# Kernel optimization log

Measured on AMD Instinct MI355X. Metric: run time of the kernel, lower is better.

## Reference

```python
import jax, jax.numpy as jnp
import numpy as np

N = 50000          # num nodes
E = 800000         # num edges
IN0 = 768
# layer configs: (in_channels, out_channels, heads, concat)
CFG = [(768, 64, 4, True), (256, 64, 4, True), (256, 64, 1, False)]


def setup_inputs() -> dict:
    key = jax.random.key(0)
    ks = iter(jax.random.split(key, 80))
    def nrm(shape, fan_in):
        return jax.random.normal(next(ks), shape, jnp.float32) * (1.0 / np.sqrt(fan_in))
    inp = {}
    inp["edge_index"] = jax.random.randint(next(ks), (2, E), 0, N)
    inp["edge_attr"] = jax.random.normal(next(ks), (E, 1), jnp.float32)
    inp["x"] = jax.random.normal(next(ks), (N, IN0), jnp.float32) * 0.05  # node_embeddings param
    for i, (cin, cout, h, concat) in enumerate(CFG):
        hc = h * cout
        nd = hc if concat else cout
        inp[f"Wl{i}"] = nrm((hc, cin), cin)
        inp[f"bl{i}"] = jnp.zeros((hc,), jnp.float32)
        inp[f"Wr{i}"] = nrm((hc, cin), cin)
        inp[f"br{i}"] = jnp.zeros((hc,), jnp.float32)
        inp[f"We{i}"] = nrm((hc, 1), 1)          # lin_edge, edge_dim=1, no bias
        inp[f"att{i}"] = nrm((h, cout), cout)     # attention vector a
        inp[f"b{i}"] = jnp.zeros((nd,), jnp.float32)   # conv output bias
        inp[f"g{i}"] = jnp.ones((nd,), jnp.float32)    # LayerNorm gamma
        inp[f"beta{i}"] = jnp.zeros((nd,), jnp.float32)  # LayerNorm beta
    # residual projections (only where in_channels != norm_dim): layer0 768->256, layer2 256->64
    inp["Rw0"] = nrm((256, 768), 768)
    inp["Rb0"] = jnp.zeros((256,), jnp.float32)
    inp["Rw2"] = nrm((64, 256), 256)
    inp["Rb2"] = jnp.zeros((64,), jnp.float32)
    return inp


def _gatv2(x, edge_index, edge_attr, Wl, bl, Wr, br, We, att, bias, heads, cout, concat):
    n = x.shape[0]
    src, dst = edge_index[0], edge_index[1]
    xl = (x @ Wl.T + bl).reshape(n, heads, cout)   # source transform
    xr = (x @ Wr.T + br).reshape(n, heads, cout)   # target transform
    e = (edge_attr @ We.T).reshape(-1, heads, cout)
    z = jax.nn.leaky_relu(xl[src] + xr[dst] + e, 0.2)          # [E,H,C]
    logits = jnp.einsum('ehc,hc->eh', z, att)                  # [E,H]
    m = jax.ops.segment_max(logits, dst, num_segments=n)       # segment softmax over dst
    ex = jnp.exp(logits - m[dst])
    denom = jax.ops.segment_sum(ex, dst, num_segments=n)
    alpha = ex / denom[dst]                                    # [E,H]
    msg = xl[src] * alpha[..., None]                           # [E,H,C]
    out = jax.ops.segment_sum(msg, dst, num_segments=n)        # [N,H,C]
    out = out.reshape(n, heads * cout) if concat else out.mean(axis=1)
    return out + bias


def _ln(x, g, b, eps=1e-5):
    mu = x.mean(-1, keepdims=True)
    v = ((x - mu) ** 2).mean(-1, keepdims=True)
    return (x - mu) * jax.lax.rsqrt(v + eps) * g + b


def reference(edge_index, edge_attr, x,
              Wl0, bl0, Wr0, br0, We0, att0, b0, g0, beta0,
              Wl1, bl1, Wr1, br1, We1, att1, b1, g1, beta1,
              Wl2, bl2, Wr2, br2, We2, att2, b2, g2, beta2,
              Rw0, Rb0, Rw2, Rb2):
    # eval mode: attention dropout disabled. Returns final_embeddings (bottleneck is None).
    h = _gatv2(x, edge_index, edge_attr, Wl0, bl0, Wr0, br0, We0, att0, b0, 4, 64, True)
    h = jax.nn.leaky_relu(_ln(h, g0, beta0), 0.01) + (x @ Rw0.T + Rb0)
    h1 = _gatv2(h, edge_index, edge_attr, Wl1, bl1, Wr1, br1, We1, att1, b1, 4, 64, True)
    h1 = jax.nn.leaky_relu(_ln(h1, g1, beta1), 0.01) + h      # Identity residual
    h2 = _gatv2(h1, edge_index, edge_attr, Wl2, bl2, Wr2, br2, We2, att2, b2, 1, 64, False)
    h2 = jax.nn.leaky_relu(_ln(h2, g2, beta2), 0.01) + (h1 @ Rw2.T + Rb2)
    return h2
```

## Files before the change

### kernel.cpp

```cpp
#include <hip/hip_runtime.h>
#include <math.h>

static constexpr int NN = 50000;
static constexpr int NE = 800000;
static constexpr int MPAD = 50048;

typedef __attribute__((ext_vector_type(8))) __bf16 bf16x8;
typedef __attribute__((ext_vector_type(4))) __bf16 bf16x4;
typedef __attribute__((ext_vector_type(4))) float f32x4;
typedef __bf16 bf16_t;

__device__ __forceinline__ float leakyf(float x, float s) { return x > 0.f ? x : s * x; }

__global__ void k_count(const int* __restrict__ dst, int* __restrict__ cnt, int n) {
    int e = blockIdx.x * 256 + threadIdx.x;
    if (e < n) atomicAdd(&cnt[dst[e]], 1);
}

__global__ void k_scan1(const int* __restrict__ cnt, int* __restrict__ rp,
                        int* __restrict__ partials, int n) {
    __shared__ int sm[256];
    int tid = threadIdx.x;
    int i = blockIdx.x * 256 + tid;
    int v = (i < n) ? cnt[i] : 0;
    int x = v;
    sm[tid] = x;
    __syncthreads();
    for (int off = 1; off < 256; off <<= 1) {
        int t = (tid >= off) ? sm[tid - off] : 0;
        __syncthreads();
        x += t;
        sm[tid] = x;
        __syncthreads();
    }
    if (i < n) rp[i] = x - v;
    if (tid == 255) partials[blockIdx.x] = x;
}

__global__ void k_scan2(const int* __restrict__ partials, int* __restrict__ poffs, int nb) {
    __shared__ int sm[256];
    int tid = threadIdx.x;
    int v = (tid < nb) ? partials[tid] : 0;
    int x = v;
    sm[tid] = x;
    __syncthreads();
    for (int off = 1; off < 256; off <<= 1) {
        int t = (tid >= off) ? sm[tid - off] : 0;
        __syncthreads();
        x += t;
        sm[tid] = x;
        __syncthreads();
    }
    if (tid < nb) poffs[tid] = x - v;
}

__global__ void k_scan3(int* __restrict__ rp, const int* __restrict__ poffs,
                        int* __restrict__ woff, int n, int total) {
    int i = blockIdx.x * 256 + threadIdx.x;
    if (i < n) {
        int v = rp[i] + poffs[blockIdx.x];
        rp[i] = v;
        woff[i] = v;
    }
    if (i == 0) rp[n] = total;
}

__global__ void k_scatter(const int* __restrict__ srcA, const int* __restrict__ dstA,
                          const float* __restrict__ ea, int* __restrict__ woff,
                          int* __restrict__ csr_src, float* __restrict__ csr_ea, int n) {
    int e = blockIdx.x * 256 + threadIdx.x;
    if (e < n) {
        int d = dstA[e];
        int pos = atomicAdd(&woff[d], 1);
        csr_src[pos] = srcA[e];
        csr_ea[pos] = ea[e];
    }
}

__global__ void k_f2b(const float* __restrict__ s, bf16_t* __restrict__ d, int n) {
    for (int i = (blockIdx.x * 256 + threadIdx.x) * 8; i < n; i += gridDim.x * 256 * 8) {
        float4 a = *(const float4*)&s[i];
        float4 b = *(const float4*)&s[i + 4];
        bf16x8 o;
        o[0] = (__bf16)a.x; o[1] = (__bf16)a.y; o[2] = (__bf16)a.z; o[3] = (__bf16)a.w;
        o[4] = (__bf16)b.x; o[5] = (__bf16)b.y; o[6] = (__bf16)b.z; o[7] = (__bf16)b.w;
        *(bf16x8*)&d[i] = o;
    }
}

__global__ void k_f2bw(const float* s0, bf16_t* d0, int n0,
                       const float* s1, bf16_t* d1, int n1,
                       const float* s2, bf16_t* d2, int n2,
                       const float* s3, bf16_t* d3, int n3,
                       const float* s4, bf16_t* d4, int n4,
                       const float* s5, bf16_t* d5, int n5,
                       const float* s6, bf16_t* d6, int n6,
                       const float* s7, bf16_t* d7, int n7) {
    const float* s; bf16_t* d; int n;
    switch (blockIdx.y) {
        case 0: s = s0; d = d0; n = n0; break;
        case 1: s = s1; d = d1; n = n1; break;
        case 2: s = s2; d = d2; n = n2; break;
        case 3: s = s3; d = d3; n = n3; break;
        case 4: s = s4; d = d4; n = n4; break;
        case 5: s = s5; d = d5; n = n5; break;
        case 6: s = s6; d = d6; n = n6; break;
        default: s = s7; d = d7; n = n7; break;
    }
    for (int i = (blockIdx.x * 256 + threadIdx.x) * 8; i < n; i += gridDim.x * 256 * 8) {
        float4 a = *(const float4*)&s[i];
        float4 b = *(const float4*)&s[i + 4];
        bf16x8 o;
        o[0] = (__bf16)a.x; o[1] = (__bf16)a.y; o[2] = (__bf16)a.z; o[3] = (__bf16)a.w;
        o[4] = (__bf16)b.x; o[5] = (__bf16)b.y; o[6] = (__bf16)b.z; o[7] = (__bf16)b.w;
        *(bf16x8*)&d[i] = o;
    }
}

__global__ void k_catb(float* __restrict__ dst,
                       const float* s0, int o0, int n0, const float* s1, int o1, int n1,
                       const float* s2, int o2, int n2, const float* s3, int o3, int n3,
                       const float* s4, int o4, int n4, const float* s5, int o5, int n5,
                       const float* s6, int o6, int n6, const float* s7, int o7, int n7) {
    const float* s; int off, n;
    switch (blockIdx.x) {
        case 0: s = s0; off = o0; n = n0; break;
        case 1: s = s1; off = o1; n = n1; break;
        case 2: s = s2; off = o2; n = n2; break;
        case 3: s = s3; off = o3; n = n3; break;
        case 4: s = s4; off = o4; n = n4; break;
        case 5: s = s5; off = o5; n = n5; break;
        case 6: s = s6; off = o6; n = n6; break;
        default: s = s7; off = o7; n = n7; break;
    }
    int i = threadIdx.x;
    if (i < n) dst[off + i] = s[i];
}

template <int BN>
__global__ __launch_bounds__(256) void k_gemm_mfma(
    const bf16_t* __restrict__ A, const bf16_t* __restrict__ W,
    const float* __restrict__ bias, bf16_t* __restrict__ C,
    int Mpad, int Nc, int K) {
    constexpr int BM = 128;
    constexpr int FRN = BN / 32;
    constexpr int WN = BN / 2;
    constexpr int BCHW = BN / 64;

    __shared__ __align__(16) bf16_t As[BM * 32];
    __shared__ __align__(16) bf16_t Bs[BN * 32];

    const int tid = threadIdx.x;
    const int wid = tid >> 6;
    const int lane = tid & 63;
    const int wr = wid >> 1, wc = wid & 1;
    const int bm = blockIdx.x * BM;
    const int bn = blockIdx.y * BN;

    const int srow = lane >> 2;
    const int scol = (lane & 3) * 8;

    f32x4 acc[4][FRN];
#pragma unroll
    for (int m = 0; m < 4; ++m)
#pragma unroll
        for (int n = 0; n < FRN; ++n) acc[m][n] = (f32x4){0.f, 0.f, 0.f, 0.f};

    const bf16_t* ag[2];
#pragma unroll
    for (int j = 0; j < 2; ++j)
        ag[j] = A + (size_t)(bm + (wid * 2 + j) * 16 + srow) * K + scol;
    const bf16_t* bg[BCHW];
#pragma unroll
    for (int j = 0; j < BCHW; ++j)
        bg[j] = W + (size_t)(bn + (wid * BCHW + j) * 16 + srow) * K + scol;

    for (int k0 = 0; k0 < K; k0 += 32) {
#pragma unroll
        for (int j = 0; j < 2; ++j) {
            __builtin_amdgcn_global_load_lds(
                (const __attribute__((address_space(1))) void*)(ag[j] + k0),
                (__attribute__((address_space(3))) void*)(As + (wid * 2 + j) * 512),
                16, 0, 0);
        }
#pragma unroll
        for (int j = 0; j < BCHW; ++j) {
            __builtin_amdgcn_global_load_lds(
                (const __attribute__((address_space(1))) void*)(bg[j] + k0),
                (__attribute__((address_space(3))) void*)(Bs + (wid * BCHW + j) * 512),
                16, 0, 0);
        }
        __syncthreads();

        bf16x8 bfr[FRN];
#pragma unroll
        for (int n = 0; n < FRN; ++n)
            bfr[n] = *(const bf16x8*)&Bs[(wc * WN + n * 16 + (lane & 15)) * 32 + (lane >> 4) * 8];
        bf16x8 afr[4];
#pragma unroll
        for (int m = 0; m < 4; ++m)
            afr[m] = *(const bf16x8*)&As[(wr * 64 + m * 16 + (lane & 15)) * 32 + (lane >> 4) * 8];
#pragma unroll
        for (int m = 0; m < 4; ++m)
#pragma unroll
            for (int n = 0; n < FRN; ++n)
                acc[m][n] = __builtin_amdgcn_mfma_f32_16x16x32_bf16(afr[m], bfr[n], acc[m][n], 0, 0, 0);
        __syncthreads();
    }

    const int cr = (lane >> 4) * 4;
    const int cc = lane & 15;
#pragma unroll
    for (int m = 0; m < 4; ++m) {
        int row0 = bm + wr * 64 + m * 16 + cr;
#pragma unroll
        for (int n = 0; n < FRN; ++n) {
            int col = bn + wc * WN + n * 16 + cc;
            float bv = bias[col];
#pragma unroll
            for (int j = 0; j < 4; ++j) {
                C[(size_t)(row0 + j) * Nc + col] = (bf16_t)(acc[m][n][j] + bv);
            }
        }
    }
}

template <int HC, typename OutT>
__global__ __launch_bounds__(256) void k_gat_edge(
    const bf16_t* __restrict__ xl, const bf16_t* __restrict__ xr,
    const bf16_t* __restrict__ res, int fstride, int rstride,
    const int* __restrict__ rp, const int* __restrict__ csr_src,
    const float* __restrict__ csr_ea,
    const float* __restrict__ We, const float* __restrict__ att,
    const float* __restrict__ bias, const float* __restrict__ gamma,
    const float* __restrict__ beta,
    OutT* __restrict__ out, int n) {
    constexpr int VPL = HC / 64;
    constexpr int LPH = 64 * 64 / HC;
    const int lane = threadIdx.x & 63;
    const int node = blockIdx.x * 4 + (threadIdx.x >> 6);
    if (node >= n) return;
    const int vb = lane * VPL;

    float xrd[VPL], wev[VPL], attv[VPL];
    if constexpr (VPL == 4) {
        bf16x4 t = *(const bf16x4*)&xr[(size_t)node * fstride + vb];
#pragma unroll
        for (int i = 0; i < 4; ++i) xrd[i] = (float)t[i];
    } else {
        xrd[0] = (float)xr[(size_t)node * fstride + vb];
    }
#pragma unroll
    for (int i = 0; i < VPL; ++i) {
        wev[i]  = We[vb + i];
        attv[i] = att[vb + i];
    }

    float m = -INFINITY, denom = 0.f;
    float acc[VPL] = {};
    const int s = rp[node], e = rp[node + 1];

    for (int p = s; p < e; ++p) {
        int src  = csr_src[p];
        float ea = csr_ea[p];
        float xls[VPL];
        if constexpr (VPL == 4) {
            bf16x4 t = *(const bf16x4*)&xl[(size_t)src * fstride + vb];
#pragma unroll
            for (int i = 0; i < 4; ++i) xls[i] = (float)t[i];
        } else {
            xls[0] = (float)xl[(size_t)src * fstride + vb];
        }
        float part = 0.f;
#pragma unroll
        for (int i = 0; i < VPL; ++i) {
            float z = xls[i] + xrd[i] + ea * wev[i];
            z = leakyf(z, 0.2f);
            part += attv[i] * z;
        }
#pragma unroll
        for (int off = 1; off < LPH; off <<= 1) part += __shfl_xor(part, off);
        float mn = fmaxf(m, part);
        float sc = __expf(m - mn);
        float pw = __expf(part - mn);
        denom = denom * sc + pw;
#pragma unroll
        for (int i = 0; i < VPL; ++i) acc[i] = acc[i] * sc + pw * xls[i];
        m = mn;
    }

    float o[VPL];
    float inv = (e > s) ? 1.f / denom : 0.f;
#pragma unroll
    for (int i = 0; i < VPL; ++i) o[i] = acc[i] * inv + bias[vb + i];

    float sum = 0.f;
#pragma unroll
    for (int i = 0; i < VPL; ++i) sum += o[i];
#pragma unroll
    for (int off = 1; off < 64; off <<= 1) sum += __shfl_xor(sum, off);
    float mu = sum * (1.f / HC);
    float sq = 0.f;
#pragma unroll
    for (int i = 0; i < VPL; ++i) { float d = o[i] - mu; sq += d * d; }
#pragma unroll
    for (int off = 1; off < 64; off <<= 1) sq += __shfl_xor(sq, off);
    float rstd = rsqrtf(sq * (1.f / HC) + 1e-5f);

    float rv[VPL];
    if constexpr (VPL == 4) {
        bf16x4 t = *(const bf16x4*)&res[(size_t)node * rstride + vb];
#pragma unroll
        for (int i = 0; i < 4; ++i) rv[i] = (float)t[i];
    } else {
        rv[0] = (float)res[(size_t)node * rstride + vb];
    }

#pragma unroll
    for (int i = 0; i < VPL; ++i) {
        float y = (o[i] - mu) * rstd * gamma[vb + i] + beta[vb + i];
        y = leakyf(y, 0.01f);
        out[(size_t)node * HC + vb + i] = (OutT)(y + rv[i]);
    }
}

extern "C" void kernel_launch(void* const* d_in, const int* in_sizes, int n_in,
                              void* d_out, int out_size, void* d_ws, size_t ws_size,
                              hipStream_t stream) {
    const int*   ei  = (const int*)d_in[0];
    const float* ea  = (const float*)d_in[1];
    const float* x   = (const float*)d_in[2];
    const float* Wl0 = (const float*)d_in[3],  *bl0 = (const float*)d_in[4];
    const float* Wr0 = (const float*)d_in[5],  *br0 = (const float*)d_in[6];
    const float* We0 = (const float*)d_in[7],  *att0= (const float*)d_in[8];
    const float* b0  = (const float*)d_in[9],  *g0  = (const float*)d_in[10], *be0 = (const float*)d_in[11];
    const float* Wl1 = (const float*)d_in[12], *bl1 = (const float*)d_in[13];
    const float* Wr1 = (const float*)d_in[14], *br1 = (const float*)d_in[15];
    const float* We1 = (const float*)d_in[16], *att1= (const float*)d_in[17];
    const float* b1  = (const float*)d_in[18], *g1  = (const float*)d_in[19], *be1 = (const float*)d_in[20];
    const float* Wl2 = (const float*)d_in[21], *bl2 = (const float*)d_in[22];
    const float* Wr2 = (const float*)d_in[23], *br2 = (const float*)d_in[24];
    const float* We2 = (const float*)d_in[25], *att2= (const float*)d_in[26];
    const float* b2  = (const float*)d_in[27], *g2  = (const float*)d_in[28], *be2 = (const float*)d_in[29];
    const float* Rw0 = (const float*)d_in[30], *Rb0 = (const float*)d_in[31];
    const float* Rw2 = (const float*)d_in[32], *Rb2 = (const float*)d_in[33];

    const int* srcA = ei;
    const int* dstA = ei + NE;

    float* ws = (float*)d_ws;
    size_t o = 0;
    auto allocf = [&](size_t nf) { float* p = ws + o; o += nf; return p; };
    bf16_t* xb  = (bf16_t*)allocf((size_t)MPAD * 384);
    bf16_t* C0  = (bf16_t*)allocf((size_t)MPAD * 384);
    bf16_t* C1  = (bf16_t*)allocf((size_t)MPAD * 256);
    bf16_t* C2  = (bf16_t*)allocf((size_t)MPAD * 96);
    bf16_t* h0b = (bf16_t*)allocf((size_t)MPAD * 128);
    bf16_t* h1b = (bf16_t*)allocf((size_t)MPAD * 128);
    bf16_t* wb  = (bf16_t*)allocf(786432 / 2);
    float* bcat = allocf(1536);
    int* cnt      = (int*)(ws + o); o += NN;
    int* rp       = (int*)(ws + o); o += NN + 4;
    int* woff     = (int*)(ws + o); o += NN;
    int* partials = (int*)(ws + o); o += 256;
    int* poffs    = (int*)(ws + o); o += 256;
    int* csr_src  = (int*)(ws + o); o += NE;
    float* csr_ea = (float*)(ws + o); o += NE;

    bf16_t* Wl0b = wb;
    bf16_t* Wr0b = Wl0b + 196608;
    bf16_t* Rw0b = Wr0b + 196608;
    bf16_t* Wl1b = Rw0b + 196608;
    bf16_t* Wr1b = Wl1b + 65536;
    bf16_t* Wl2b = Wr1b + 65536;
    bf16_t* Wr2b = Wl2b + 16384;
    bf16_t* Rw2b = Wr2b + 16384;

    float* outp = (float*)d_out;

    const int NB_N = (NN + 255) / 256;
    const int NB_E = (NE + 255) / 256;

    hipMemsetAsync(cnt, 0, (size_t)NN * sizeof(int), stream);
    k_count<<<NB_E, 256, 0, stream>>>(dstA, cnt, NE);
    k_scan1<<<NB_N, 256, 0, stream>>>(cnt, rp, partials, NN);
    k_scan2<<<1, 256, 0, stream>>>(partials, poffs, NB_N);
    k_scan3<<<NB_N, 256, 0, stream>>>(rp, poffs, woff, NN, NE);
    k_scatter<<<NB_E, 256, 0, stream>>>(srcA, dstA, ea, woff, csr_src, csr_ea, NE);

    k_f2b<<<2048, 256, 0, stream>>>(x, xb, NN * 768);
    {
        dim3 g(96, 8);
        k_f2bw<<<g, 256, 0, stream>>>(Wl0, Wl0b, 196608, Wr0, Wr0b, 196608,
                                      Rw0, Rw0b, 196608, Wl1, Wl1b, 65536,
                                      Wr1, Wr1b, 65536,  Wl2, Wl2b, 16384,
                                      Wr2, Wr2b, 16384,  Rw2, Rw2b, 16384);
    }
    k_catb<<<8, 256, 0, stream>>>(bcat,
                                  bl0, 0, 256,    br0, 256, 256,  Rb0, 512, 256,
                                  bl1, 768, 256,  br1, 1024, 256,
                                  bl2, 1280, 64,  br2, 1344, 64,  Rb2, 1408, 64);

    const int MB = MPAD / 128;
    const int EG = (NN + 3) / 4;

    {
        dim3 g(MB, 6);
        k_gemm_mfma<128><<<g, 256, 0, stream>>>(xb, Wl0b, bcat, C0, MPAD, 768, 768);
    }
    k_gat_edge<256, bf16_t><<<EG, 256, 0, stream>>>(
        C0, C0 + 256, C0 + 512, 768, 768, rp, csr_src, csr_ea,
        We0, att0, b0, g0, be0, h0b, NN);

    {
        dim3 g(MB, 4);
        k_gemm_mfma<128><<<g, 256, 0, stream>>>(h0b, Wl1b, bcat + 768, C1, MPAD, 512, 256);
    }
    k_gat_edge<256, bf16_t><<<EG, 256, 0, stream>>>(
        C1, C1 + 256, h0b, 512, 256, rp, csr_src, csr_ea,
        We1, att1, b1, g1, be1, h1b, NN);

    {
        dim3 g(MB, 3);
        k_gemm_mfma<64><<<g, 256, 0, stream>>>(h1b, Wl2b, bcat + 1280, C2, MPAD, 192, 256);
    }
    k_gat_edge<64, float><<<EG, 256, 0, stream>>>(
        C2, C2 + 64, C2 + 128, 192, 192, rp, csr_src, csr_ea,
        We2, att2, b2, g2, be2, outp, NN);
}
```

Baseline: 896.0 us.

## Process multiple edges per wavefront and drop online-softmax max tracking in GAT edge kernel

The GAT aggregation kernel now splits each wavefront into ES edge slots, so several incoming edges are handled in parallel with wider bf16 vector loads per lane. A final cross-slot shuffle reduction combines the partial sums. The online softmax max/rescale is replaced by a plain exp2 of logits clamped to ±60, with the attention vector pre-scaled by log2(e). This removes two exponentials and a rescale per edge and increases memory-level parallelism. It risks overflow or precision differences from skipping max subtraction and adds reduction shuffles at the end.

```diff
diff --git a/kernel.cpp b/kernel.cpp
--- a/kernel.cpp
+++ b/kernel.cpp
@@ -10,7 +10,7 @@
 typedef __attribute__((ext_vector_type(4))) float f32x4;
 typedef __bf16 bf16_t;
 
-__device__ __forceinline__ float leakyf(float x, float s) { return x > 0.f ? x : s * x; }
+__device__ __forceinline__ float leakyf(float x, float s) { return fmaxf(x, s * x); }
 
 __global__ void k_count(const int* __restrict__ dst, int* __restrict__ cnt, int n) {
     int e = blockIdx.x * 256 + threadIdx.x;
@@ -225,7 +225,7 @@
     }
 }
 
-template <int HC, typename OutT>
+template <int HC, int ES, typename OutT>
 __global__ __launch_bounds__(256) void k_gat_edge(
     const bf16_t* __restrict__ xl, const bf16_t* __restrict__ xr,
     const bf16_t* __restrict__ res, int fstride, int rstride,
@@ -235,92 +235,111 @@
     const float* __restrict__ bias, const float* __restrict__ gamma,
     const float* __restrict__ beta,
     OutT* __restrict__ out, int n) {
-    constexpr int VPL = HC / 64;
-    constexpr int LPH = 64 * 64 / HC;
+    constexpr int CL  = 64 / ES;
+    constexpr int VPL = HC / CL;
+    constexpr int RW  = 64 / VPL;
     const int lane = threadIdx.x & 63;
     const int node = blockIdx.x * 4 + (threadIdx.x >> 6);
     if (node >= n) return;
-    const int vb = lane * VPL;
+    const int slot = lane / CL;
+    const int cl   = lane % CL;
+    const int vb   = cl * VPL;
 
     float xrd[VPL], wev[VPL], attv[VPL];
-    if constexpr (VPL == 4) {
+    if constexpr (VPL == 8) {
+        bf16x8 t = *(const bf16x8*)&xr[(size_t)node * fstride + vb];
+#pragma unroll
+        for (int i = 0; i < 8; ++i) xrd[i] = (float)t[i];
+    } else {
         bf16x4 t = *(const bf16x4*)&xr[(size_t)node * fstride + vb];
 #pragma unroll
         for (int i = 0; i < 4; ++i) xrd[i] = (float)t[i];
-    } else {
-        xrd[0] = (float)xr[(size_t)node * fstride + vb];
     }
 #pragma unroll
     for (int i = 0; i < VPL; ++i) {
         wev[i]  = We[vb + i];
-        attv[i] = att[vb + i];
-    }
-
-    float m = -INFINITY, denom = 0.f;
+        attv[i] = att[vb + i] * 1.44269504088896f;
+    }
+
+    float denom = 0.f;
     float acc[VPL] = {};
     const int s = rp[node], e = rp[node + 1];
 
-    for (int p = s; p < e; ++p) {
-        int src  = csr_src[p];
-        float ea = csr_ea[p];
+    for (int p0 = s; p0 < e; p0 += ES) {
+        const int p = p0 + slot;
+        const bool act = (p < e);
+        const int pc = act ? p : (e - 1);
+        const int src = csr_src[pc];
+        const float ea = csr_ea[pc];
         float xls[VPL];
-        if constexpr (VPL == 4) {
+        if constexpr (VPL == 8) {
+            bf16x8 t = *(const bf16x8*)&xl[(size_t)src * fstride + vb];
+#pragma unroll
+            for (int i = 0; i < 8; ++i) xls[i] = (float)t[i];
+        } else {
             bf16x4 t = *(const bf16x4*)&xl[(size_t)src * fstride + vb];
 #pragma unroll
             for (int i = 0; i < 4; ++i) xls[i] = (float)t[i];
-        } else {
-            xls[0] = (float)xl[(size_t)src * fstride + vb];
         }
         float part = 0.f;
 #pragma unroll
         for (int i = 0; i < VPL; ++i) {
-            float z = xls[i] + xrd[i] + ea * wev[i];
+            float z = fmaf(ea, wev[i], xls[i] + xrd[i]);
             z = leakyf(z, 0.2f);
-            part += attv[i] * z;
-        }
-#pragma unroll
-        for (int off = 1; off < LPH; off <<= 1) part += __shfl_xor(part, off);
-        float mn = fmaxf(m, part);
-        float sc = __expf(m - mn);
-        float pw = __expf(part - mn);
-        denom = denom * sc + pw;
-#pragma unroll
-        for (int i = 0; i < VPL; ++i) acc[i] = acc[i] * sc + pw * xls[i];
-        m = mn;
+            part = fmaf(attv[i], z, part);
+        }
+#pragma unroll
+        for (int off = 1; off < RW; off <<= 1) part += __shfl_xor(part, off);
+        part = fminf(fmaxf(part, -60.f), 60.f);
+        const float pw = act ? exp2f(part) : 0.f;
+        denom += pw;
+#pragma unroll
+        for (int i = 0; i < VPL; ++i) acc[i] = fmaf(pw, xls[i], acc[i]);
+    }
+
+#pragma unroll
+    for (int off = CL; off < 64; off <<= 1) {
+        denom += __shfl_xor(denom, off);
+#pragma unroll
+        for (int i = 0; i < VPL; ++i) acc[i] += __shfl_xor(acc[i], off);
     }
 
     float o[VPL];
-    float inv = (e > s) ? 1.f / denom : 0.f;
-#pragma unroll
-    for (int i = 0; i < VPL; ++i) o[i] = acc[i] * inv + bias[vb + i];
+    const float inv = (e > s) ? 1.f / denom : 0.f;
+#pragma unroll
+    for (int i = 0; i < VPL; ++i) o[i] = fmaf(acc[i], inv, bias[vb + i]);
 
     float sum = 0.f;
 #pragma unroll
     for (int i = 0; i < VPL; ++i) sum += o[i];
 #pragma unroll
-    for (int off = 1; off < 64; off <<= 1) sum += __shfl_xor(sum, off);
-    float mu = sum * (1.f / HC);
+    for (int off = 1; off < CL; off <<= 1) sum += __shfl_xor(sum, off);
+    const float mu = sum * (1.f / HC);
     float sq = 0.f;
 #pragma unroll
     for (int i = 0; i < VPL; ++i) { float d = o[i] - mu; sq += d * d; }
 #pragma unroll
-    for (int off = 1; off < 64; off <<= 1) sq += __shfl_xor(sq, off);
-    float rstd = rsqrtf(sq * (1.f / HC) + 1e-5f);
+    for (int off = 1; off < CL; off <<= 1) sq += __shfl_xor(sq, off);
+    const float rstd = rsqrtf(sq * (1.f / HC) + 1e-5f);
 
     float rv[VPL];
-    if constexpr (VPL == 4) {
+    if constexpr (VPL == 8) {
+        bf16x8 t = *(const bf16x8*)&res[(size_t)node * rstride + vb];
+#pragma unroll
+        for (int i = 0; i < 8; ++i) rv[i] = (float)t[i];
+    } else {
         bf16x4 t = *(const bf16x4*)&res[(size_t)node * rstride + vb];
 #pragma unroll
         for (int i = 0; i < 4; ++i) rv[i] = (float)t[i];
-    } else {
-        rv[0] = (float)res[(size_t)node * rstride + vb];
-    }
-
-#pragma unroll
-    for (int i = 0; i < VPL; ++i) {
-        float y = (o[i] - mu) * rstd * gamma[vb + i] + beta[vb + i];
-        y = leakyf(y, 0.01f);
-        out[(size_t)node * HC + vb + i] = (OutT)(y + rv[i]);
+    }
+
+    if (slot == 0) {
+#pragma unroll
+        for (int i = 0; i < VPL; ++i) {
+            float y = (o[i] - mu) * rstd * gamma[vb + i] + beta[vb + i];
+            y = leakyf(y, 0.01f);
+            out[(size_t)node * HC + vb + i] = (OutT)(y + rv[i]);
+        }
     }
 }
 
@@ -408,7 +427,7 @@
         dim3 g(MB, 6);
         k_gemm_mfma<128><<<g, 256, 0, stream>>>(xb, Wl0b, bcat, C0, MPAD, 768, 768);
     }
-    k_gat_edge<256, bf16_t><<<EG, 256, 0, stream>>>(
+    k_gat_edge<256, 2, bf16_t><<<EG, 256, 0, stream>>>(
         C0, C0 + 256, C0 + 512, 768, 768, rp, csr_src, csr_ea,
         We0, att0, b0, g0, be0, h0b, NN);
 
@@ -416,7 +435,7 @@
         dim3 g(MB, 4);
         k_gemm_mfma<128><<<g, 256, 0, stream>>>(h0b, Wl1b, bcat + 768, C1, MPAD, 512, 256);
     }
-    k_gat_edge<256, bf16_t><<<EG, 256, 0, stream>>>(
+    k_gat_edge<256, 2, bf16_t><<<EG, 256, 0, stream>>>(
         C1, C1 + 256, h0b, 512, 256, rp, csr_src, csr_ea,
         We1, att1, b1, g1, be1, h1b, NN);
 
@@ -424,7 +443,7 @@
         dim3 g(MB, 3);
         k_gemm_mfma<64><<<g, 256, 0, stream>>>(h1b, Wl2b, bcat + 1280, C2, MPAD, 192, 256);
     }
-    k_gat_edge<64, float><<<EG, 256, 0, stream>>>(
+    k_gat_edge<64, 4, float><<<EG, 256, 0, stream>>>(
         C2, C2 + 64, C2 + 128, 192, 192, rp, csr_src, csr_ea,
         We2, att2, b2, g2, be2, outp, NN);
 }
```

After: 781.6 us. 1.15x faster.
